# Kernel tuning notes

Hardware: AMD Instinct MI355X
Metric: run time of the kernel (lower is better)

The kernel has to match this reference:

```python
import jax, jax.numpy as jnp
import numpy as np

B = 512; H = 84; W = 84; K = 20; DEPTH = 24; EMB = 512
FCS = 7 * 7 * 64
FLOW_C = 0.01


def _init(key, shape, fan_in):
    return jax.random.normal(key, shape, jnp.float32) * (1.0 / np.sqrt(fan_in))


def setup_inputs() -> dict:
    key = jax.random.key(0)
    ks = jax.random.split(key, 22)
    return {
        "inp": jax.random.normal(ks[0], (B, 2, H, W), jnp.float32),
        "cw1": _init(ks[1], (32, 2, 8, 8), 2 * 8 * 8),
        "cb1": jnp.zeros((32,), jnp.float32),
        "cw2": _init(ks[2], (64, 32, 4, 4), 32 * 4 * 4),
        "cb2": jnp.zeros((64,), jnp.float32),
        "cw3": _init(ks[3], (64, 64, 3, 3), 64 * 3 * 3),
        "cb3": jnp.zeros((64,), jnp.float32),
        "fcw": _init(ks[4], (EMB, FCS), FCS),
        "fcb": jnp.zeros((EMB,), jnp.float32),
        "otw": _init(ks[5], (K * 2, EMB), EMB),
        "otb": jnp.zeros((K * 2,), jnp.float32),
        "ctw": _init(ks[6], (2, EMB), EMB),
        "ctb": jnp.zeros((2,), jnp.float32),
        "m1w": _init(ks[7], (21 * 21 * DEPTH, EMB), EMB),
        "m1b": jnp.zeros((21 * 21 * DEPTH,), jnp.float32),
        "c1w": _init(ks[8], (DEPTH, DEPTH, 3, 3), DEPTH * 9),
        "c1b": jnp.zeros((DEPTH,), jnp.float32),
        "c2w": _init(ks[9], (DEPTH, DEPTH, 3, 3), DEPTH * 9),
        "c2b": jnp.zeros((DEPTH,), jnp.float32),
        "c3w": _init(ks[10], (K, DEPTH, 1, 1), DEPTH),
        "c3b": jnp.zeros((K,), jnp.float32),
    }


def _conv(x, w, b, stride, pad):
    y = jax.lax.conv_general_dilated(
        x, w, (stride, stride), [(pad, pad), (pad, pad)],
        dimension_numbers=("NCHW", "OIHW", "NCHW"))
    return y + b[None, :, None, None]


def _up_mat(in_s, out_s):
    # bilinear, align_corners=True (torch UpsamplingBilinear2d)
    pos = jnp.arange(out_s, dtype=jnp.float32) * ((in_s - 1) / (out_s - 1))
    lo = jnp.clip(jnp.floor(pos).astype(jnp.int32), 0, in_s - 2)
    w = pos - lo.astype(jnp.float32)
    r = jnp.arange(out_s)
    M = jnp.zeros((out_s, in_s), jnp.float32)
    M = M.at[r, lo].add(1.0 - w).at[r, lo + 1].add(w)
    return M


def reference(inp, cw1, cb1, cw2, cb2, cw3, cb3, fcw, fcb, otw, otb,
              ctw, ctb, m1w, m1b, c1w, c1b, c2w, c2b, c3w, c3b):
    bs = inp.shape[0]
    # CNN encoder
    h1 = jax.nn.relu(_conv(inp, cw1, cb1, 4, 0))
    h2 = jax.nn.relu(_conv(h1, cw2, cb2, 2, 0))
    h3 = jax.nn.relu(_conv(h2, cw3, cb3, 1, 0))
    feat = h3.reshape(bs, -1)                              # [B, 3136]
    x = jax.nn.relu(feat @ fcw.T + fcb)                    # [B, EMB]
    # mask decoder
    m = (x @ m1w.T + m1b).reshape(bs, DEPTH, 21, 21)
    M42 = _up_mat(21, 42)
    m = jnp.einsum('bchw,Hh,Ww->bcHW', m, M42, M42)        # 21->42
    m = jax.nn.relu(m + _conv(m, c1w, c1b, 1, 1))
    M84 = _up_mat(42, 84)
    m = jnp.einsum('bchw,Hh,Ww->bcHW', m, M84, M84)        # 42->84
    m = jax.nn.relu(m + _conv(m, c2w, c2b, 1, 1))
    m = jax.nn.sigmoid(_conv(m, c3w, c3b, 1, 0))           # [B, K, 84, 84]
    # per-object translations -> flow
    ot = (x @ otw.T + otb).reshape(bs, K, 2)
    flow = jnp.einsum('bkhw,bkt->bthw', m, ot).reshape(bs, 2, H * W)
    ct = (x @ ctw.T + ctb)[:, :, None]                     # [B,2,1]
    flat_flow = flow + ct
    img_size_f = FLOW_C * jnp.array([[float(H)], [float(W)]], jnp.float32)
    # mesh grid: row 0 = y (row index), row 1 = x (col index)
    gy = jnp.repeat(jnp.arange(H, dtype=jnp.float32), W)
    gx = jnp.tile(jnp.arange(W, dtype=jnp.float32), H)
    grid = jnp.stack([gy, gx], 0)                          # [2, H*W]
    coords = img_size_f * flat_flow + grid
    ys = coords[:, 0, :].reshape(-1)                       # [B*H*W]
    xs = coords[:, 1, :].reshape(-1)
    # manual bilinear gather from second input frame
    src = inp[:, 1, :, :].reshape(-1)                      # [B*H*W] flat image
    x0 = jnp.clip(jnp.floor(xs).astype(jnp.int32), 0, W - 1)
    x1 = jnp.clip(x0 + 1, 0, W - 1)
    y0 = jnp.clip(jnp.floor(ys).astype(jnp.int32), 0, H - 1)
    y1 = jnp.clip(y0 + 1, 0, H - 1)
    base = jnp.repeat(jnp.arange(bs, dtype=jnp.int32) * (H * W), H * W)
    Ia = src[base + y0 * W + x0]
    Ib = src[base + y1 * W + x0]
    Ic = src[base + y0 * W + x1]
    Id = src[base + y1 * W + x1]
    xc = jnp.clip(xs, 0.0, float(W - 1))
    yc = jnp.clip(ys, 0.0, float(H - 1))
    x0f = x0.astype(jnp.float32); x1f = x1.astype(jnp.float32)
    y0f = y0.astype(jnp.float32); y1f = y1.astype(jnp.float32)
    out = ((x1f - xc) * (y1f - yc) * Ia + (x1f - xc) * (yc - y0f) * Ib +
           (xc - x0f) * (y1f - yc) * Ic + (xc - x0f) * (yc - y0f) * Id)
    return out.reshape(bs, 1, H, W)
```

## Files before the change

### kernel.cpp

```cpp
#include <hip/hip_runtime.h>
#include <math.h>

namespace {

typedef float f32x2 __attribute__((ext_vector_type(2)));

#if defined(__has_builtin)
#if __has_builtin(__builtin_elementwise_fma)
#define HAVE_EW_FMA 1
#endif
#endif

__device__ __forceinline__ f32x2 pkfma(f32x2 a, f32x2 b, f32x2 c) {
#ifdef HAVE_EW_FMA
  return __builtin_elementwise_fma(a, b, c);
#else
  return a * b + c;
#endif
}

constexpr int IMS  = 84;
constexpr int NPIX = IMS * IMS;
constexpr int KOBJ = 20;

constexpr size_t OFF_X    = 0;
constexpr size_t OFF_OT   = 262144;
constexpr size_t OFF_CT   = 282624;
constexpr size_t OFF_WT2  = 283648;
constexpr size_t OFF_WT3  = 316416;
constexpr size_t OFF_M0   = 353280;
constexpr size_t OFF_R1   = 5772288;
constexpr size_t OFF_H1   = OFF_R1;
constexpr size_t OFF_H2   = 12325888;
constexpr size_t OFF_FEAT = 14980096;

__global__ void transpose_w(const float* __restrict__ w, float* __restrict__ wt,
                            int OC, int CKK) {
  int idx = blockIdx.x * 256 + threadIdx.x;
  if (idx < OC * CKK) {
    int oc = idx / CKK, ckk = idx % CKK;
    wt[ckk * OC + oc] = w[idx];
  }
}

__global__ __launch_bounds__(256) void conv1_k(
    const float* __restrict__ inp, const float* __restrict__ w,
    const float* __restrict__ bias, float* __restrict__ out) {
  __shared__ __align__(16) float sIn[NPIX];
  __shared__ __align__(16) float sW[128 * 32];
  const int b = blockIdx.x, t = threadIdx.x;
  for (int i = t; i < 4096; i += 256) {
    int oc = i >> 7, ckk = i & 127;
    sW[ckk * 32 + oc] = w[i];
  }
  const float* ip = inp + (size_t)b * 2 * NPIX;
  const int oc0 = (t & 7) * 4;
  const int pg  = t >> 3;
  int ibase[13];
#pragma unroll
  for (int k = 0; k < 13; k++) {
    int p = pg + 32 * k; if (p > 399) p = 399;
    ibase[k] = (p / 20) * 4 * 84 + (p % 20) * 4;
  }
  f32x2 acc[13][2];
#pragma unroll
  for (int k = 0; k < 13; k++) { acc[k][0] = f32x2{0.f, 0.f}; acc[k][1] = f32x2{0.f, 0.f}; }
  for (int c = 0; c < 2; c++) {
    __syncthreads();
    for (int i = t; i < NPIX; i += 256) sIn[i] = ip[c * NPIX + i];
    __syncthreads();
    for (int u = 0; u < 8; u++) {
#pragma unroll
      for (int v = 0; v < 8; v++) {
        const float4 wv = *(const float4*)&sW[((c * 8 + u) * 8 + v) * 32 + oc0];
        const f32x2 w0 = {wv.x, wv.y}, w1 = {wv.z, wv.w};
        const int off = u * 84 + v;
#pragma unroll
        for (int k = 0; k < 13; k++) {
          float x = sIn[off + ibase[k]];
          f32x2 xv = {x, x};
          acc[k][0] = pkfma(w0, xv, acc[k][0]);
          acc[k][1] = pkfma(w1, xv, acc[k][1]);
        }
      }
    }
  }
  float b0 = bias[oc0], b1 = bias[oc0+1], b2 = bias[oc0+2], b3 = bias[oc0+3];
  float* op = out + (size_t)b * 32 * 400;
#pragma unroll
  for (int k = 0; k < 13; k++) {
    int p = pg + 32 * k;
    if (p < 400) {
      op[(oc0+0)*400 + p] = fmaxf(acc[k][0][0] + b0, 0.f);
      op[(oc0+1)*400 + p] = fmaxf(acc[k][0][1] + b1, 0.f);
      op[(oc0+2)*400 + p] = fmaxf(acc[k][1][0] + b2, 0.f);
      op[(oc0+3)*400 + p] = fmaxf(acc[k][1][1] + b3, 0.f);
    }
  }
}

__global__ __launch_bounds__(256) void conv2_k(
    const float* __restrict__ in, const float* __restrict__ wt,
    const float* __restrict__ bias, float* __restrict__ out) {
  __shared__ float sIn[32 * 400];
  const int b = blockIdx.x, t = threadIdx.x;
  const float* ip = in + (size_t)b * 12800;
  for (int i = t; i < 12800; i += 256) sIn[i] = ip[i];
  __syncthreads();
  const int oc0 = (t & 7) * 8;
  const int pg  = t >> 3;
  int base[3];
#pragma unroll
  for (int k = 0; k < 3; k++) {
    int p = pg + 32 * k; if (p > 80) p = 80;
    base[k] = (p / 9) * 40 + (p % 9) * 2;
  }
  f32x2 acc[3][4];
#pragma unroll
  for (int k = 0; k < 3; k++)
#pragma unroll
    for (int o = 0; o < 4; o++) acc[k][o] = f32x2{0.f, 0.f};
  for (int c = 0; c < 32; c++) {
#pragma unroll
    for (int u = 0; u < 4; u++)
#pragma unroll
      for (int v = 0; v < 4; v++) {
        const float* wp = wt + ((c * 4 + u) * 4 + v) * 64 + oc0;
        float4 wa = *(const float4*)wp;
        float4 wb = *(const float4*)(wp + 4);
        const f32x2 w0 = {wa.x, wa.y}, w1 = {wa.z, wa.w};
        const f32x2 w2 = {wb.x, wb.y}, w3 = {wb.z, wb.w};
        int off = c * 400 + u * 20 + v;
#pragma unroll
        for (int k = 0; k < 3; k++) {
          float x = sIn[off + base[k]];
          f32x2 xv = {x, x};
          acc[k][0] = pkfma(w0, xv, acc[k][0]);
          acc[k][1] = pkfma(w1, xv, acc[k][1]);
          acc[k][2] = pkfma(w2, xv, acc[k][2]);
          acc[k][3] = pkfma(w3, xv, acc[k][3]);
        }
      }
  }
  float* op = out + (size_t)b * 5184;
#pragma unroll
  for (int k = 0; k < 3; k++) {
    int p = pg + 32 * k;
    if (p < 81) {
#pragma unroll
      for (int o = 0; o < 8; o++)
        op[(oc0+o)*81 + p] = fmaxf(acc[k][o >> 1][o & 1] + bias[oc0+o], 0.f);
    }
  }
}

__global__ __launch_bounds__(256) void conv3_k(
    const float* __restrict__ in, const float* __restrict__ wt,
    const float* __restrict__ bias, float* __restrict__ out) {
  __shared__ float sIn[64 * 81];
  const int b = blockIdx.x, t = threadIdx.x;
  const float* ip = in + (size_t)b * 5184;
  for (int i = t; i < 5184; i += 256) sIn[i] = ip[i];
  __syncthreads();
  const int oc0 = (t & 7) * 8;
  const int pg  = t >> 3;
  int base[2];
#pragma unroll
  for (int k = 0; k < 2; k++) {
    int p = pg + 32 * k; if (p > 48) p = 48;
    base[k] = (p / 7) * 9 + (p % 7);
  }
  f32x2 acc[2][4];
#pragma unroll
  for (int k = 0; k < 2; k++)
#pragma unroll
    for (int o = 0; o < 4; o++) acc[k][o] = f32x2{0.f, 0.f};
  for (int c = 0; c < 64; c++) {
#pragma unroll
    for (int u = 0; u < 3; u++)
#pragma unroll
      for (int v = 0; v < 3; v++) {
        const float* wp = wt + ((c * 3 + u) * 3 + v) * 64 + oc0;
        float4 wa = *(const float4*)wp;
        float4 wb = *(const float4*)(wp + 4);
        const f32x2 w0 = {wa.x, wa.y}, w1 = {wa.z, wa.w};
        const f32x2 w2 = {wb.x, wb.y}, w3 = {wb.z, wb.w};
        int off = c * 81 + u * 9 + v;
#pragma unroll
        for (int k = 0; k < 2; k++) {
          float x = sIn[off + base[k]];
          f32x2 xv = {x, x};
          acc[k][0] = pkfma(w0, xv, acc[k][0]);
          acc[k][1] = pkfma(w1, xv, acc[k][1]);
          acc[k][2] = pkfma(w2, xv, acc[k][2]);
          acc[k][3] = pkfma(w3, xv, acc[k][3]);
        }
      }
  }
  float* op = out + (size_t)b * 3136;
#pragma unroll
  for (int k = 0; k < 2; k++) {
    int p = pg + 32 * k;
    if (p < 49) {
#pragma unroll
      for (int o = 0; o < 8; o++)
        op[(oc0+o)*49 + p] = fmaxf(acc[k][o >> 1][o & 1] + bias[oc0+o], 0.f);
    }
  }
}

template<bool RELU>
__global__ __launch_bounds__(256) void gemm_k(
    const float* __restrict__ A, const float* __restrict__ Wm,
    const float* __restrict__ bias, float* __restrict__ C,
    int N, int K) {
  __shared__ __align__(16) float As[16][68];
  __shared__ __align__(16) float Ws[16][68];
  const int t = threadIdx.x;
  const int m0 = blockIdx.y * 64, n0 = blockIdx.x * 64;
  const int r  = t >> 2;
  const int kq = (t & 3) * 4;
  const int r0 = (t >> 4) * 4, c0 = (t & 15) * 4;
  f32x2 acc[4][2];
#pragma unroll
  for (int i = 0; i < 4; i++) { acc[i][0] = f32x2{0.f, 0.f}; acc[i][1] = f32x2{0.f, 0.f}; }
  for (int k0 = 0; k0 < K; k0 += 16) {
    float4 a = *(const float4*)(A + (size_t)(m0 + r) * K + k0 + kq);
    int wrow = n0 + r;
    float4 wv = make_float4(0.f, 0.f, 0.f, 0.f);
    if (wrow < N) wv = *(const float4*)(Wm + (size_t)wrow * K + k0 + kq);
    __syncthreads();
    As[kq+0][r] = a.x; As[kq+1][r] = a.y; As[kq+2][r] = a.z; As[kq+3][r] = a.w;
    Ws[kq+0][r] = wv.x; Ws[kq+1][r] = wv.y; Ws[kq+2][r] = wv.z; Ws[kq+3][r] = wv.w;
    __syncthreads();
#pragma unroll
    for (int kk = 0; kk < 16; kk++) {
      float4 av = *(const float4*)&As[kk][r0];
      float4 bv = *(const float4*)&Ws[kk][c0];
      const f32x2 b0 = {bv.x, bv.y}, b1 = {bv.z, bv.w};
      float ar[4] = {av.x, av.y, av.z, av.w};
#pragma unroll
      for (int i = 0; i < 4; i++) {
        f32x2 ai = {ar[i], ar[i]};
        acc[i][0] = pkfma(b0, ai, acc[i][0]);
        acc[i][1] = pkfma(b1, ai, acc[i][1]);
      }
    }
  }
#pragma unroll
  for (int i = 0; i < 4; i++) {
    int row = m0 + r0 + i;
#pragma unroll
    for (int j = 0; j < 4; j++) {
      int col = n0 + c0 + j;
      if (col < N) {
        float v = acc[i][j >> 1][j & 1] + bias[col];
        C[(size_t)row * N + col] = RELU ? fmaxf(v, 0.f) : v;
      }
    }
  }
}

__global__ __launch_bounds__(256) void gemm_splitk_k(
    const float* __restrict__ A, const float* __restrict__ Wm,
    float* __restrict__ Cpart, int N, int K, int Kslice) {
  __shared__ __align__(16) float As[16][68];
  __shared__ __align__(16) float Ws[16][68];
  const int t = threadIdx.x;
  const int m0 = blockIdx.y * 64, n0 = blockIdx.x * 64;
  const int kbeg = blockIdx.z * Kslice;
  const int kend = kbeg + Kslice;
  const int r  = t >> 2;
  const int kq = (t & 3) * 4;
  const int r0 = (t >> 4) * 4, c0 = (t & 15) * 4;
  f32x2 acc[4][2];
#pragma unroll
  for (int i = 0; i < 4; i++) { acc[i][0] = f32x2{0.f, 0.f}; acc[i][1] = f32x2{0.f, 0.f}; }
  for (int k0 = kbeg; k0 < kend; k0 += 16) {
    float4 a = *(const float4*)(A + (size_t)(m0 + r) * K + k0 + kq);
    float4 wv = *(const float4*)(Wm + (size_t)(n0 + r) * K + k0 + kq);
    __syncthreads();
    As[kq+0][r] = a.x; As[kq+1][r] = a.y; As[kq+2][r] = a.z; As[kq+3][r] = a.w;
    Ws[kq+0][r] = wv.x; Ws[kq+1][r] = wv.y; Ws[kq+2][r] = wv.z; Ws[kq+3][r] = wv.w;
    __syncthreads();
#pragma unroll
    for (int kk = 0; kk < 16; kk++) {
      float4 av = *(const float4*)&As[kk][r0];
      float4 bv = *(const float4*)&Ws[kk][c0];
      const f32x2 b0 = {bv.x, bv.y}, b1 = {bv.z, bv.w};
      float ar[4] = {av.x, av.y, av.z, av.w};
#pragma unroll
      for (int i = 0; i < 4; i++) {
        f32x2 ai = {ar[i], ar[i]};
        acc[i][0] = pkfma(b0, ai, acc[i][0]);
        acc[i][1] = pkfma(b1, ai, acc[i][1]);
      }
    }
  }
  float* cp = Cpart + (size_t)blockIdx.z * 512 * 512;
#pragma unroll
  for (int i = 0; i < 4; i++) {
    int row = m0 + r0 + i;
#pragma unroll
    for (int j = 0; j < 4; j++)
      cp[(size_t)row * N + n0 + c0 + j] = acc[i][j >> 1][j & 1];
  }
}

__global__ __launch_bounds__(256) void splitk_reduce_k(
    const float* __restrict__ Cpart, const float* __restrict__ bias,
    float* __restrict__ X) {
  int i4 = blockIdx.x * 256 + threadIdx.x;
  if (i4 < 65536) {
    int col4 = (i4 & 127) * 4;
    float4 p0 = *(const float4*)&Cpart[(size_t)i4 * 4];
    float4 p1 = *(const float4*)&Cpart[262144 + (size_t)i4 * 4];
    float4 p2 = *(const float4*)&Cpart[524288 + (size_t)i4 * 4];
    float4 p3 = *(const float4*)&Cpart[786432 + (size_t)i4 * 4];
    float4 bb = *(const float4*)&bias[col4];
    float4 o;
    o.x = fmaxf(p0.x + p1.x + p2.x + p3.x + bb.x, 0.f);
    o.y = fmaxf(p0.y + p1.y + p2.y + p3.y + bb.y, 0.f);
    o.z = fmaxf(p0.z + p1.z + p2.z + p3.z + bb.z, 0.f);
    o.w = fmaxf(p0.w + p1.w + p2.w + p3.w + bb.w, 0.f);
    *(float4*)&X[(size_t)i4 * 4] = o;
  }
}

__global__ __launch_bounds__(256) void gemm128_k(
    const float* __restrict__ A, const float* __restrict__ Wm,
    const float* __restrict__ bias, float* __restrict__ C,
    int N, int K) {
  __shared__ __align__(16) float As[16][132];
  __shared__ __align__(16) float Ws[16][132];
  const int t = threadIdx.x;
  const int m0 = blockIdx.y * 128, n0 = blockIdx.x * 128;
  const int lr = t >> 1;
  const int kq = (t & 1) * 8;
  const int r0 = (t >> 4) * 8, c0 = (t & 15) * 8;
  f32x2 acc[8][4];
#pragma unroll
  for (int i = 0; i < 8; i++)
#pragma unroll
    for (int j = 0; j < 4; j++) acc[i][j] = f32x2{0.f, 0.f};
  for (int k0 = 0; k0 < K; k0 += 16) {
    const float* ap = A + (size_t)(m0 + lr) * K + k0 + kq;
    float4 a0 = *(const float4*)ap;
    float4 a1 = *(const float4*)(ap + 4);
    int wrow = n0 + lr;
    float4 w0 = make_float4(0.f,0.f,0.f,0.f), w1 = make_float4(0.f,0.f,0.f,0.f);
    if (wrow < N) {
      const float* wp = Wm + (size_t)wrow * K + k0 + kq;
      w0 = *(const float4*)wp;
      w1 = *(const float4*)(wp + 4);
    }
    __syncthreads();
    As[kq+0][lr] = a0.x; As[kq+1][lr] = a0.y; As[kq+2][lr] = a0.z; As[kq+3][lr] = a0.w;
    As[kq+4][lr] = a1.x; As[kq+5][lr] = a1.y; As[kq+6][lr] = a1.z; As[kq+7][lr] = a1.w;
    Ws[kq+0][lr] = w0.x; Ws[kq+1][lr] = w0.y; Ws[kq+2][lr] = w0.z; Ws[kq+3][lr] = w0.w;
    Ws[kq+4][lr] = w1.x; Ws[kq+5][lr] = w1.y; Ws[kq+6][lr] = w1.z; Ws[kq+7][lr] = w1.w;
    __syncthreads();
#pragma unroll
    for (int kk = 0; kk < 16; kk++) {
      float4 av0 = *(const float4*)&As[kk][r0];
      float4 av1 = *(const float4*)&As[kk][r0 + 4];
      float4 bv0 = *(const float4*)&Ws[kk][c0];
      float4 bv1 = *(const float4*)&Ws[kk][c0 + 4];
      float ar[8] = {av0.x, av0.y, av0.z, av0.w, av1.x, av1.y, av1.z, av1.w};
      f32x2 br[4] = {{bv0.x, bv0.y}, {bv0.z, bv0.w}, {bv1.x, bv1.y}, {bv1.z, bv1.w}};
#pragma unroll
      for (int i = 0; i < 8; i++) {
        f32x2 ai = {ar[i], ar[i]};
#pragma unroll
        for (int j = 0; j < 4; j++) acc[i][j] = pkfma(br[j], ai, acc[i][j]);
      }
    }
  }
#pragma unroll
  for (int i = 0; i < 8; i++) {
    int row = m0 + r0 + i;
#pragma unroll
    for (int j = 0; j < 8; j++) {
      int col = n0 + c0 + j;
      if (col < N)
        C[(size_t)row * N + col] = acc[i][j >> 1][j & 1] + bias[col];
    }
  }
}

__global__ __launch_bounds__(384, 6) void upconv1_k(
    const float* __restrict__ X, const float* __restrict__ wt,
    const float* __restrict__ bias, float* __restrict__ out) {
  constexpr int S_IN = 21, S_OUT = 42, TR = 6, UH = 8, UW = 44, NTILE = 7;
  __shared__ __align__(16) float sU[24 * UH * UW];
  const int b = blockIdx.x / NTILE;
  const int y0 = (blockIdx.x % NTILE) * TR;
  const int t = threadIdx.x;
  const float* xb = X + (size_t)b * 24 * S_IN * S_IN;
  const float sc = (float)(S_IN - 1) / (float)(S_OUT - 1);
  for (int rr = t; rr < UH * UW; rr += 384) {
    const int ry = rr / UW, cx = rr % UW;
    const int y = y0 + ry - 1, x = cx - 1;
    float* sdst = &sU[rr];
    if (y >= 0 && y < S_OUT && x >= 0 && x < S_OUT) {
      float py = y * sc, px = x * sc;
      int ly = (int)py; if (ly > S_IN - 2) ly = S_IN - 2;
      int lx = (int)px; if (lx > S_IN - 2) lx = S_IN - 2;
      float wy = py - (float)ly, wx = px - (float)lx;
      const f32x2 wxv = {wx, wx};
      const float* xc = xb + ly * S_IN + lx;
      for (int c = 0; c < 24; c++) {
        f32x2 a  = {xc[0], xc[S_IN]};
        f32x2 bb = {xc[1], xc[S_IN + 1]};
        f32x2 h = pkfma(wxv, bb - a, a);
        *sdst = h[0] + wy * (h[1] - h[0]);
        xc += S_IN * S_IN;
        sdst += UH * UW;
      }
    } else {
      for (int c = 0; c < 24; c++) { *sdst = 0.f; sdst += UH * UW; }
    }
  }
  __syncthreads();
  if (t < 252) {
    const int ry = t / 42, lx = t % 42;
    f32x2 acc[12];
#pragma unroll
    for (int j = 0; j < 12; j++) acc[j] = f32x2{0.f, 0.f};
    for (int ic = 0; ic < 24; ic++) {
      const float* urow = &sU[(ic * UH + ry) * UW + lx];
      const float* wp = wt + ic * 216;
#pragma unroll
      for (int ky = 0; ky < 3; ky++) {
        float x0v = urow[ky * UW + 0];
        float x1v = urow[ky * UW + 1];
        float x2v = urow[ky * UW + 2];
        f32x2 X0 = {x0v, x0v}, X1 = {x1v, x1v}, X2 = {x2v, x2v};
        const f32x2* wk2 = (const f32x2*)(wp + ky * 72);
#pragma unroll
        for (int j = 0; j < 12; j++)
          acc[j] = pkfma(wk2[j], X0,
                   pkfma(wk2[12 + j], X1,
                   pkfma(wk2[24 + j], X2, acc[j])));
      }
    }
    const int yy = y0 + ry;
#pragma unroll
    for (int j = 0; j < 12; j++) {
      f32x2 u2 = { sU[((2*j)   * UH + ry + 1) * UW + lx + 1],
                   sU[((2*j+1) * UH + ry + 1) * UW + lx + 1] };
      f32x2 b2 = *(const f32x2*)&bias[2*j];
      f32x2 s = u2 + acc[j] + b2;
      out[(((size_t)b * 24 + 2*j    ) * S_OUT + yy) * S_OUT + lx] = fmaxf(s[0], 0.f);
      out[(((size_t)b * 24 + 2*j + 1) * S_OUT + yy) * S_OUT + lx] = fmaxf(s[1], 0.f);
    }
  }
}

__global__ __launch_bounds__(384, 6) void upconv2_final_k(
    const float* __restrict__ R1, const float* __restrict__ inp,
    const float* __restrict__ wt, const float* __restrict__ bias,
    const float* __restrict__ c3w, const float* __restrict__ c3b,
    const float* __restrict__ ot, const float* __restrict__ ct,
    float* __restrict__ out) {
  constexpr int S_IN = 42, S_OUT = 84, TR = 6, UH = 8, TW = 42, UW = 44;
  __shared__ __align__(16) float sU[24 * UH * UW];
  const int blk = blockIdx.x;
  const int b = blk / 28;
  const int rr0 = blk % 28;
  const int y0 = (rr0 >> 1) * TR;
  const int x0 = (rr0 & 1) * TW;
  const int t = threadIdx.x;
  const float* xb = R1 + (size_t)b * 24 * S_IN * S_IN;
  const float sc = (float)(S_IN - 1) / (float)(S_OUT - 1);
  for (int rr = t; rr < UH * UW; rr += 384) {
    const int ry = rr / UW, cx = rr % UW;
    const int y = y0 + ry - 1, x = x0 + cx - 1;
    float* sdst = &sU[rr];
    if (y >= 0 && y < S_OUT && x >= 0 && x < S_OUT) {
      float py = y * sc, px = x * sc;
      int ly = (int)py; if (ly > S_IN - 2) ly = S_IN - 2;
      int lx = (int)px; if (lx > S_IN - 2) lx = S_IN - 2;
      float wy = py - (float)ly, wx = px - (float)lx;
      const f32x2 wxv = {wx, wx};
      const float* xc = xb + ly * S_IN + lx;
      for (int c = 0; c < 24; c++) {
        f32x2 a  = {xc[0], xc[S_IN]};
        f32x2 bb = {xc[1], xc[S_IN + 1]};
        f32x2 h = pkfma(wxv, bb - a, a);
        *sdst = h[0] + wy * (h[1] - h[0]);
        xc += S_IN * S_IN;
        sdst += UH * UW;
      }
    } else {
      for (int c = 0; c < 24; c++) { *sdst = 0.f; sdst += UH * UW; }
    }
  }
  __syncthreads();
  if (t < 252) {
    const int ry = t / 42, lx = t % 42;
    f32x2 acc[12];
#pragma unroll
    for (int j = 0; j < 12; j++) acc[j] = f32x2{0.f, 0.f};
    for (int ic = 0; ic < 24; ic++) {
      const float* urow = &sU[(ic * UH + ry) * UW + lx];
      const float* wp = wt + ic * 216;
#pragma unroll
      for (int ky = 0; ky < 3; ky++) {
        float x0v = urow[ky * UW + 0];
        float x1v = urow[ky * UW + 1];
        float x2v = urow[ky * UW + 2];
        f32x2 X0 = {x0v, x0v}, X1 = {x1v, x1v}, X2 = {x2v, x2v};
        const f32x2* wk2 = (const f32x2*)(wp + ky * 72);
#pragma unroll
        for (int j = 0; j < 12; j++)
          acc[j] = pkfma(wk2[j], X0,
                   pkfma(wk2[12 + j], X1,
                   pkfma(wk2[24 + j], X2, acc[j])));
      }
    }
    f32x2 r[12];
#pragma unroll
    for (int j = 0; j < 12; j++) {
      f32x2 u2 = { sU[((2*j)   * UH + ry + 1) * UW + lx + 1],
                   sU[((2*j+1) * UH + ry + 1) * UW + lx + 1] };
      f32x2 b2 = *(const f32x2*)&bias[2*j];
      f32x2 s = u2 + acc[j] + b2;
      r[j][0] = fmaxf(s[0], 0.f);
      r[j][1] = fmaxf(s[1], 0.f);
    }
    f32x2 f2 = *(const f32x2*)&ct[b * 2];
    const f32x2* ot2 = (const f32x2*)(ot + b * 2 * KOBJ);
    for (int k = 0; k < KOBJ; k++) {
      f32x2 zv = {c3b[k], 0.f};
      const f32x2* cw2 = (const f32x2*)(c3w + k * 24);
#pragma unroll
      for (int j = 0; j < 12; j++) zv = pkfma(r[j], cw2[j], zv);
      float z = zv[0] + zv[1];
      float m = 1.f / (1.f + __expf(-z));
      f32x2 mv = {m, m};
      f2 = pkfma(mv, ot2[k], f2);
    }
    const int gy = y0 + ry, gx = x0 + lx;
    const float imgf = 0.01f * 84.0f;
    float ys = imgf * f2[0] + (float)gy;
    float xs = imgf * f2[1] + (float)gx;
    int ix0 = (int)floorf(xs); ix0 = ix0 < 0 ? 0 : (ix0 > 83 ? 83 : ix0);
    int iy0 = (int)floorf(ys); iy0 = iy0 < 0 ? 0 : (iy0 > 83 ? 83 : iy0);
    int ix1 = ix0 + 1 > 83 ? 83 : ix0 + 1;
    int iy1 = iy0 + 1 > 83 ? 83 : iy0 + 1;
    float xc = fminf(fmaxf(xs, 0.f), 83.f);
    float yc = fminf(fmaxf(ys, 0.f), 83.f);
    float wx1 = (float)ix1 - xc, wx0 = xc - (float)ix0;
    float wy1 = (float)iy1 - yc, wy0 = yc - (float)iy0;
    const float* src = inp + ((size_t)b * 2 + 1) * NPIX;
    float Ia = src[iy0 * 84 + ix0], Ib = src[iy1 * 84 + ix0];
    float Ic = src[iy0 * 84 + ix1], Id = src[iy1 * 84 + ix1];
    out[(size_t)b * NPIX + gy * 84 + gx] =
        wx1 * wy1 * Ia + wx1 * wy0 * Ib + wx0 * wy1 * Ic + wx0 * wy0 * Id;
  }
}

}

extern "C" void kernel_launch(void* const* d_in, const int* in_sizes, int n_in,
                              void* d_out, int out_size, void* d_ws, size_t ws_size,
                              hipStream_t stream) {
  const float* inp = (const float*)d_in[0];
  const float* cw1 = (const float*)d_in[1];
  const float* cb1 = (const float*)d_in[2];
  const float* cw2 = (const float*)d_in[3];
  const float* cb2 = (const float*)d_in[4];
  const float* cw3 = (const float*)d_in[5];
  const float* cb3 = (const float*)d_in[6];
  const float* fcw = (const float*)d_in[7];
  const float* fcb = (const float*)d_in[8];
  const float* otw = (const float*)d_in[9];
  const float* otb = (const float*)d_in[10];
  const float* ctw = (const float*)d_in[11];
  const float* ctb = (const float*)d_in[12];
  const float* m1w = (const float*)d_in[13];
  const float* m1b = (const float*)d_in[14];
  const float* c1w = (const float*)d_in[15];
  const float* c1b = (const float*)d_in[16];
  const float* c2w = (const float*)d_in[17];
  const float* c2b = (const float*)d_in[18];
  const float* c3w = (const float*)d_in[19];
  const float* c3b = (const float*)d_in[20];
  float* W = (float*)d_ws;
  float* out = (float*)d_out;

  transpose_w<<<(64 * 512 + 255) / 256, 256, 0, stream>>>(cw2, W + OFF_WT2, 64, 512);
  transpose_w<<<(64 * 576 + 255) / 256, 256, 0, stream>>>(cw3, W + OFF_WT3, 64, 576);
  conv1_k<<<512, 256, 0, stream>>>(inp, cw1, cb1, W + OFF_H1);
  conv2_k<<<512, 256, 0, stream>>>(W + OFF_H1, W + OFF_WT2, cb2, W + OFF_H2);
  conv3_k<<<512, 256, 0, stream>>>(W + OFF_H2, W + OFF_WT3, cb3, W + OFF_FEAT);
  transpose_w<<<(24 * 216 + 255) / 256, 256, 0, stream>>>(c1w, W + OFF_WT2, 24, 216);
  transpose_w<<<(24 * 216 + 255) / 256, 256, 0, stream>>>(c2w, W + OFF_WT3, 24, 216);
  gemm_splitk_k<<<dim3(8, 8, 4), 256, 0, stream>>>(W + OFF_FEAT, fcw, W + OFF_M0,
                                                   512, 3136, 784);
  splitk_reduce_k<<<256, 256, 0, stream>>>(W + OFF_M0, fcb, W + OFF_X);
  gemm_k<false><<<dim3(1, 8), 256, 0, stream>>>(W + OFF_X, otw, otb, W + OFF_OT, 40, 512);
  gemm_k<false><<<dim3(1, 8), 256, 0, stream>>>(W + OFF_X, ctw, ctb, W + OFF_CT, 2, 512);
  gemm128_k<<<dim3(83, 4), 256, 0, stream>>>(W + OFF_X, m1w, m1b, W + OFF_M0, 10584, 512);
  upconv1_k<<<512 * 7, 384, 0, stream>>>(W + OFF_M0, W + OFF_WT2, c1b, W + OFF_R1);
  upconv2_final_k<<<512 * 28, 384, 0, stream>>>(W + OFF_R1, inp, W + OFF_WT3, c2b,
                                                c3w, c3b, W + OFF_OT, W + OFF_CT, out);
}
```

Baseline: 1.103 ms.

## Switch upsample intermediates to channel-last layout with vectorized bilinear gathers

Adds a kernel that permutes the m1 weight rows and bias so the big GEMM writes its output channel-last, as [pixel][24 channels]. upconv1 then writes its output channel-last as well. Both upsample stages can now gather the four bilinear neighbours as float4 loads across channels, instead of scalar loads strided by channel planes. The cost is an extra copy of the roughly 22 MB weight matrix on every call, and scattered stores into LDS.

```diff
diff --git a/kernel.cpp b/kernel.cpp
--- a/kernel.cpp
+++ b/kernel.cpp
@@ -4,6 +4,7 @@
 namespace {
 
 typedef float f32x2 __attribute__((ext_vector_type(2)));
+typedef float f32x4 __attribute__((ext_vector_type(4)));
 
 #if defined(__has_builtin)
 #if __has_builtin(__builtin_elementwise_fma)
@@ -12,6 +13,13 @@
 #endif
 
 __device__ __forceinline__ f32x2 pkfma(f32x2 a, f32x2 b, f32x2 c) {
+#ifdef HAVE_EW_FMA
+  return __builtin_elementwise_fma(a, b, c);
+#else
+  return a * b + c;
+#endif
+}
+__device__ __forceinline__ f32x4 fma4(f32x4 a, f32x4 b, f32x4 c) {
 #ifdef HAVE_EW_FMA
   return __builtin_elementwise_fma(a, b, c);
 #else
@@ -33,6 +41,8 @@
 constexpr size_t OFF_H1   = OFF_R1;
 constexpr size_t OFF_H2   = 12325888;
 constexpr size_t OFF_FEAT = 14980096;
+constexpr size_t OFF_M1WT = OFF_H1;
+constexpr size_t OFF_M1BT = OFF_H1 + 5419008;
 
 __global__ void transpose_w(const float* __restrict__ w, float* __restrict__ wt,
                             int OC, int CKK) {
@@ -41,6 +51,18 @@
     int oc = idx / CKK, ckk = idx % CKK;
     wt[ckk * OC + oc] = w[idx];
   }
+}
+
+__global__ __launch_bounds__(128) void permute_m1(
+    const float* __restrict__ m1w, const float* __restrict__ m1b,
+    float* __restrict__ wT, float* __restrict__ bT) {
+  const int n = blockIdx.x;
+  const int c = n / 441, rem = n % 441;
+  const int np = rem * 24 + c;
+  const float4* src = (const float4*)(m1w + (size_t)n * 512);
+  float4* dst = (float4*)(wT + (size_t)np * 512);
+  dst[threadIdx.x] = src[threadIdx.x];
+  if (threadIdx.x == 0) bT[np] = m1b[n];
 }
 
 __global__ __launch_bounds__(256) void conv1_k(
@@ -390,7 +412,7 @@
 
 __global__ __launch_bounds__(384, 6) void upconv1_k(
     const float* __restrict__ X, const float* __restrict__ wt,
-    const float* __restrict__ bias, float* __restrict__ out) {
+    const float* __restrict__ bias, float* __restrict__ outT) {
   constexpr int S_IN = 21, S_OUT = 42, TR = 6, UH = 8, UW = 44, NTILE = 7;
   __shared__ __align__(16) float sU[24 * UH * UW];
   const int b = blockIdx.x / NTILE;
@@ -407,18 +429,26 @@
       int ly = (int)py; if (ly > S_IN - 2) ly = S_IN - 2;
       int lx = (int)px; if (lx > S_IN - 2) lx = S_IN - 2;
       float wy = py - (float)ly, wx = px - (float)lx;
-      const f32x2 wxv = {wx, wx};
-      const float* xc = xb + ly * S_IN + lx;
-      for (int c = 0; c < 24; c++) {
-        f32x2 a  = {xc[0], xc[S_IN]};
-        f32x2 bb = {xc[1], xc[S_IN + 1]};
-        f32x2 h = pkfma(wxv, bb - a, a);
-        *sdst = h[0] + wy * (h[1] - h[0]);
-        xc += S_IN * S_IN;
-        sdst += UH * UW;
+      const f32x4 wx4 = {wx, wx, wx, wx};
+      const f32x4 wy4 = {wy, wy, wy, wy};
+      const float* p00 = xb + ((size_t)ly * S_IN + lx) * 24;
+#pragma unroll
+      for (int g = 0; g < 6; g++) {
+        f32x4 q00 = *(const f32x4*)(p00 + 4 * g);
+        f32x4 q01 = *(const f32x4*)(p00 + 24 + 4 * g);
+        f32x4 q10 = *(const f32x4*)(p00 + 24 * S_IN + 4 * g);
+        f32x4 q11 = *(const f32x4*)(p00 + 24 * S_IN + 24 + 4 * g);
+        f32x4 ht = fma4(wx4, q01 - q00, q00);
+        f32x4 hb = fma4(wx4, q11 - q10, q10);
+        f32x4 v  = fma4(wy4, hb - ht, ht);
+        sdst[(4*g + 0) * UH * UW] = v[0];
+        sdst[(4*g + 1) * UH * UW] = v[1];
+        sdst[(4*g + 2) * UH * UW] = v[2];
+        sdst[(4*g + 3) * UH * UW] = v[3];
       }
     } else {
-      for (int c = 0; c < 24; c++) { *sdst = 0.f; sdst += UH * UW; }
+#pragma unroll
+      for (int c = 0; c < 24; c++) sdst[c * UH * UW] = 0.f;
     }
   }
   __syncthreads();
@@ -445,20 +475,25 @@
       }
     }
     const int yy = y0 + ry;
-#pragma unroll
-    for (int j = 0; j < 12; j++) {
-      f32x2 u2 = { sU[((2*j)   * UH + ry + 1) * UW + lx + 1],
-                   sU[((2*j+1) * UH + ry + 1) * UW + lx + 1] };
-      f32x2 b2 = *(const f32x2*)&bias[2*j];
-      f32x2 s = u2 + acc[j] + b2;
-      out[(((size_t)b * 24 + 2*j    ) * S_OUT + yy) * S_OUT + lx] = fmaxf(s[0], 0.f);
-      out[(((size_t)b * 24 + 2*j + 1) * S_OUT + yy) * S_OUT + lx] = fmaxf(s[1], 0.f);
+    float* orow = outT + ((size_t)b * 1764 + yy * 42 + lx) * 24;
+#pragma unroll
+    for (int g = 0; g < 6; g++) {
+      f32x4 u = { sU[((4*g + 0) * UH + ry + 1) * UW + lx + 1],
+                  sU[((4*g + 1) * UH + ry + 1) * UW + lx + 1],
+                  sU[((4*g + 2) * UH + ry + 1) * UW + lx + 1],
+                  sU[((4*g + 3) * UH + ry + 1) * UW + lx + 1] };
+      f32x4 a = {acc[2*g][0], acc[2*g][1], acc[2*g+1][0], acc[2*g+1][1]};
+      f32x4 bb = *(const f32x4*)&bias[4*g];
+      f32x4 s = u + a + bb;
+      s[0] = fmaxf(s[0], 0.f); s[1] = fmaxf(s[1], 0.f);
+      s[2] = fmaxf(s[2], 0.f); s[3] = fmaxf(s[3], 0.f);
+      *(f32x4*)(orow + 4*g) = s;
     }
   }
 }
 
 __global__ __launch_bounds__(384, 6) void upconv2_final_k(
-    const float* __restrict__ R1, const float* __restrict__ inp,
+    const float* __restrict__ R1T, const float* __restrict__ inp,
     const float* __restrict__ wt, const float* __restrict__ bias,
     const float* __restrict__ c3w, const float* __restrict__ c3b,
     const float* __restrict__ ot, const float* __restrict__ ct,
@@ -471,7 +506,7 @@
   const int y0 = (rr0 >> 1) * TR;
   const int x0 = (rr0 & 1) * TW;
   const int t = threadIdx.x;
-  const float* xb = R1 + (size_t)b * 24 * S_IN * S_IN;
+  const float* xb = R1T + (size_t)b * 1764 * 24;
   const float sc = (float)(S_IN - 1) / (float)(S_OUT - 1);
   for (int rr = t; rr < UH * UW; rr += 384) {
     const int ry = rr / UW, cx = rr % UW;
@@ -482,18 +517,26 @@
       int ly = (int)py; if (ly > S_IN - 2) ly = S_IN - 2;
       int lx = (int)px; if (lx > S_IN - 2) lx = S_IN - 2;
       float wy = py - (float)ly, wx = px - (float)lx;
-      const f32x2 wxv = {wx, wx};
-      const float* xc = xb + ly * S_IN + lx;
-      for (int c = 0; c < 24; c++) {
-        f32x2 a  = {xc[0], xc[S_IN]};
-        f32x2 bb = {xc[1], xc[S_IN + 1]};
-        f32x2 h = pkfma(wxv, bb - a, a);
-        *sdst = h[0] + wy * (h[1] - h[0]);
-        xc += S_IN * S_IN;
-        sdst += UH * UW;
+      const f32x4 wx4 = {wx, wx, wx, wx};
+      const f32x4 wy4 = {wy, wy, wy, wy};
+      const float* p00 = xb + ((size_t)ly * S_IN + lx) * 24;
+#pragma unroll
+      for (int g = 0; g < 6; g++) {
+        f32x4 q00 = *(const f32x4*)(p00 + 4 * g);
+        f32x4 q01 = *(const f32x4*)(p00 + 24 + 4 * g);
+        f32x4 q10 = *(const f32x4*)(p00 + 24 * S_IN + 4 * g);
+        f32x4 q11 = *(const f32x4*)(p00 + 24 * S_IN + 24 + 4 * g);
+        f32x4 ht = fma4(wx4, q01 - q00, q00);
+        f32x4 hb = fma4(wx4, q11 - q10, q10);
+        f32x4 v  = fma4(wy4, hb - ht, ht);
+        sdst[(4*g + 0) * UH * UW] = v[0];
+        sdst[(4*g + 1) * UH * UW] = v[1];
+        sdst[(4*g + 2) * UH * UW] = v[2];
+        sdst[(4*g + 3) * UH * UW] = v[3];
       }
     } else {
-      for (int c = 0; c < 24; c++) { *sdst = 0.f; sdst += UH * UW; }
+#pragma unroll
+      for (int c = 0; c < 24; c++) sdst[c * UH * UW] = 0.f;
     }
   }
   __syncthreads();
@@ -594,6 +637,7 @@
   transpose_w<<<(64 * 576 + 255) / 256, 256, 0, stream>>>(cw3, W + OFF_WT3, 64, 576);
   conv1_k<<<512, 256, 0, stream>>>(inp, cw1, cb1, W + OFF_H1);
   conv2_k<<<512, 256, 0, stream>>>(W + OFF_H1, W + OFF_WT2, cb2, W + OFF_H2);
+  permute_m1<<<10584, 128, 0, stream>>>(m1w, m1b, W + OFF_M1WT, W + OFF_M1BT);
   conv3_k<<<512, 256, 0, stream>>>(W + OFF_H2, W + OFF_WT3, cb3, W + OFF_FEAT);
   transpose_w<<<(24 * 216 + 255) / 256, 256, 0, stream>>>(c1w, W + OFF_WT2, 24, 216);
   transpose_w<<<(24 * 216 + 255) / 256, 256, 0, stream>>>(c2w, W + OFF_WT3, 24, 216);
@@ -602,7 +646,8 @@
   splitk_reduce_k<<<256, 256, 0, stream>>>(W + OFF_M0, fcb, W + OFF_X);
   gemm_k<false><<<dim3(1, 8), 256, 0, stream>>>(W + OFF_X, otw, otb, W + OFF_OT, 40, 512);
   gemm_k<false><<<dim3(1, 8), 256, 0, stream>>>(W + OFF_X, ctw, ctb, W + OFF_CT, 2, 512);
-  gemm128_k<<<dim3(83, 4), 256, 0, stream>>>(W + OFF_X, m1w, m1b, W + OFF_M0, 10584, 512);
+  gemm128_k<<<dim3(83, 4), 256, 0, stream>>>(W + OFF_X, W + OFF_M1WT, W + OFF_M1BT,
+                                             W + OFF_M0, 10584, 512);
   upconv1_k<<<512 * 7, 384, 0, stream>>>(W + OFF_M0, W + OFF_WT2, c1b, W + OFF_R1);
   upconv2_final_k<<<512 * 28, 384, 0, stream>>>(W + OFF_R1, inp, W + OFF_WT3, c2b,
                                                 c3w, c3b, W + OFF_OT, W + OFF_CT, out);
```

New measurement: 1.076 ms. -2.4%, faster.
